# Performance work log

Measured on AMD Instinct MI355X. Metric: run time of the kernel, lower is better.

The kernel has to match this reference:

```python
import jax, jax.numpy as jnp
import numpy as np

N = 1024  # batch


def setup_inputs() -> dict:
    key = jax.random.key(0)
    ks = jax.random.split(key, 10)
    meta_feature = jax.random.uniform(ks[0], (N, 6), dtype=jnp.float32)
    tile_wall_feature = jax.random.uniform(ks[1], (N, 34, 5), dtype=jnp.float32)
    tile_prep = jax.random.uniform(ks[2], (N, 320, 34, 7), dtype=jnp.float32)
    # keep tile_hidden_ct (channel 4) away from 0 so the division stays well-conditioned
    tile_prep = tile_prep.at[..., 4].add(0.5)
    fan_prep = jax.random.uniform(ks[3], (N, 320, 80), dtype=jnp.float32)
    redundant_tile_prep = jax.random.uniform(ks[4], (N, 320, 34), dtype=jnp.float32)
    count_prep = jax.random.uniform(ks[5], (N, 320), dtype=jnp.float32)
    chi_peng_count_remain = jax.random.uniform(ks[6], (N, 320), dtype=jnp.float32)
    # learned params: Linear(11,1) of TileProbModuleNew, fan_coeff, tile_coeff
    W_throw = jax.random.normal(ks[7], (11,), dtype=jnp.float32) * 0.05
    b_throw = jnp.array(0.5, dtype=jnp.float32)  # keeps prob_throw > 0 (faithful math; avoids NaN from neg**frac)
    fan_coeff = 0.1 + 0.015 * jax.random.normal(ks[8], (80,), dtype=jnp.float32)
    tile_coeff = 1.0 + 0.015 * jax.random.normal(ks[9], (34,), dtype=jnp.float32)
    fan_coeff_multiplier = jnp.ones((80,), dtype=jnp.float32).at[33].set(21.0)
    return {
        'meta_feature': meta_feature,
        'tile_wall_feature': tile_wall_feature,
        'tile_prep': tile_prep,
        'fan_prep': fan_prep,
        'redundant_tile_prep': redundant_tile_prep,
        'count_prep': count_prep,
        'chi_peng_count_remain': chi_peng_count_remain,
        'W_throw': W_throw,
        'b_throw': b_throw,
        'fan_coeff': fan_coeff,
        'fan_coeff_multiplier': fan_coeff_multiplier,
        'tile_coeff': tile_coeff,
    }


def reference(meta_feature, tile_wall_feature, tile_prep, fan_prep,
              redundant_tile_prep, count_prep, chi_peng_count_remain,
              W_throw, b_throw, fan_coeff, fan_coeff_multiplier, tile_coeff):
    n = meta_feature.shape[0]
    # TileProbModuleNew: per-tile Linear(11,1)
    meta_exp = jnp.broadcast_to(meta_feature[:, None, :], (n, 34, 6))
    feat = jnp.concatenate([meta_exp, tile_wall_feature], axis=-1)        # (n,34,11)
    prob_throw = feat @ W_throw + b_throw                                  # (n,34)

    tile_self_draw_baseline = tile_prep[..., 0]
    tile_need_count = tile_prep[..., 1]
    tile_cp_coeff = tile_prep[..., 2]
    tile_cp_base = tile_prep[..., 3]
    tile_hidden_ct = tile_prep[..., 4]
    tile_cp_switch = tile_prep[..., 5]
    tile_null_filler = tile_prep[..., 6]

    fan_pref = fan_prep * fan_coeff * fan_coeff_multiplier                 # (n,320,80)
    multiplied_fan_pref = jnp.sum(fan_pref, axis=-1)                       # (n,320)

    term1 = tile_self_draw_baseline * prob_throw[:, None, :] ** tile_need_count
    term2 = jnp.nan_to_num(tile_cp_base * tile_cp_coeff / tile_hidden_ct)
    terms_summed = term1 + tile_null_filler + term2 * tile_cp_switch      # (n,320,34)

    final_prob_throw = jnp.prod(terms_summed, axis=-1) * 100.0 * multiplied_fan_pref  # (n,320)

    redundant_prob = redundant_tile_prep * final_prob_throw[..., None]    # (n,320,34)
    redundant_prob = redundant_prob.reshape(n, 5, 64, 34)
    tile_bound_winrate = redundant_prob.sum(axis=2)                        # (n,5,34)

    weighted_tile_prob = (tile_bound_winrate * tile_coeff)[:, 0]           # (n,34)

    final_prob_ops = final_prob_throw.reshape(n, 5, 64).sum(axis=-1)       # (n,5)
    max_tile_prob_for_action = jnp.max(tile_bound_winrate, axis=2)         # (n,5)
    max_tile_prob_for_action = max_tile_prob_for_action.at[:, 0].set(final_prob_ops[:, 0])
    return (max_tile_prob_for_action, weighted_tile_prob)
```

## Files before the change

### kernel.cpp

```cpp
#include <hip/hip_runtime.h>
#include <math.h>

#define N_OPS 320

__global__ __launch_bounds__(256) void mahjong_kernel(
    const float* __restrict__ meta,
    const float* __restrict__ wall,
    const float* __restrict__ tile_prep,
    const float* __restrict__ fan_prep,
    const float* __restrict__ redundant,
    const float* __restrict__ W_throw,
    const float* __restrict__ b_throw,
    const float* __restrict__ fan_coeff,
    const float* __restrict__ fan_mult,
    const float* __restrict__ tile_coeff,
    float* __restrict__ out_max,
    float* __restrict__ out_weighted,
    int n)
{
    const int blk  = blockIdx.x;
    const int b    = blk / 5;
    const int g    = blk % 5;
    const int tid  = threadIdx.x;
    const int wave = tid >> 6;
    const int lane = tid & 63;

    __shared__ float terms_sm[32 * 34];
    __shared__ float qp_sm[32 * 21];
    __shared__ float prob_sm[34];
    __shared__ float fc_sm[80];
    __shared__ float final_sm[32];
    __shared__ float acc_sm[4][34];

    if (tid < 34) {
        float acc = b_throw[0];
        #pragma unroll
        for (int j = 0; j < 6; ++j) acc += meta[(size_t)b * 6 + j] * W_throw[j];
        const float* w = wall + ((size_t)b * 34 + tid) * 5;
        #pragma unroll
        for (int j = 0; j < 5; ++j) acc += w[j] * W_throw[6 + j];
        prob_sm[tid] = acc;
    }
    if (tid >= 64 && tid < 144) {
        int f = tid - 64;
        fc_sm[f] = fan_coeff[f] * fan_mult[f];
    }
    __syncthreads();

    float acc3 = 0.0f;
    float fsum_part = 0.0f;

    const int t_init = tid % 34;

    for (int c = 0; c < 2; ++c) {
        const size_t row0 = (size_t)b * N_OPS + g * 64 + c * 32;

        if (c) __syncthreads();

        {
            const float* tp0 = tile_prep + row0 * 238;
            int t = t_init;
            #pragma unroll
            for (int k = 0; k < 4; ++k) {
                const int tau = tid + 256 * k;
                const float* e = tp0 + 7 * tau;
                float c0 = e[0], c1 = e[1], c2 = e[2], c3 = e[3];
                float c4 = e[4], c5 = e[5], c6 = e[6];
                float term = c0 * exp2f(c1 * log2f(prob_sm[t])) + c6 + (c3 * c2 / c4) * c5;
                terms_sm[tau] = term;
                t += 18; if (t >= 34) t -= 34;
            }
            if (tid < 64) {
                const int tau = 1024 + tid;
                int t2 = tid + 4;
                if (t2 >= 34) t2 -= 34;
                if (t2 >= 34) t2 -= 34;
                const float* e = tp0 + 7 * tau;
                float c0 = e[0], c1 = e[1], c2 = e[2], c3 = e[3];
                float c4 = e[4], c5 = e[5], c6 = e[6];
                float term = c0 * exp2f(c1 * log2f(prob_sm[t2])) + c6 + (c3 * c2 / c4) * c5;
                terms_sm[tau] = term;
            }
        }

        {
            const float4* fsrc = (const float4*)(fan_prep + row0 * 80);
            #pragma unroll
            for (int k = 0; k < 3; ++k) {
                const int i = tid + 256 * k;
                if (i < 640) {
                    float4 v = fsrc[i];
                    const int r = i / 20;
                    const int q = i - r * 20;
                    const int f = 4 * q;
                    qp_sm[r * 21 + q] = v.x * fc_sm[f]     + v.y * fc_sm[f + 1]
                                      + v.z * fc_sm[f + 2] + v.w * fc_sm[f + 3];
                }
            }
        }
        __syncthreads();

        if (tid < 32) {
            const float* tr = terms_sm + tid * 34;
            float p = 1.0f;
            #pragma unroll
            for (int t = 0; t < 34; ++t) p *= tr[t];
            const float* qr = qp_sm + tid * 21;
            float q = 0.0f;
            #pragma unroll
            for (int j = 0; j < 20; ++j) q += qr[j];
            float fin = p * 100.0f * q;
            final_sm[tid] = fin;
            fsum_part += fin;
        }
        __syncthreads();

        if (lane < 34) {
            const float* rr0 = redundant + (row0 + wave * 8) * 34;
            #pragma unroll
            for (int i = 0; i < 8; ++i)
                acc3 += rr0[i * 34 + lane] * final_sm[wave * 8 + i];
        }
    }

    if (lane < 34) acc_sm[wave][lane] = acc3;
    __syncthreads();

    if (wave == 0) {
        float tbw = 0.0f;
        if (lane < 34)
            tbw = acc_sm[0][lane] + acc_sm[1][lane] + acc_sm[2][lane] + acc_sm[3][lane];
        if (g == 0) {
            if (lane < 34)
                out_weighted[(size_t)b * 34 + lane] = tbw * tile_coeff[lane];
            float fs = fsum_part;
            #pragma unroll
            for (int sh = 1; sh < 64; sh <<= 1) fs += __shfl_xor(fs, sh);
            if (lane == 0) out_max[(size_t)b * 5] = fs;
        } else {
            float m = (lane < 34) ? tbw : -INFINITY;
            #pragma unroll
            for (int sh = 1; sh < 64; sh <<= 1) m = fmaxf(m, __shfl_xor(m, sh));
            if (lane == 0) out_max[(size_t)b * 5 + g] = m;
        }
    }
}

extern "C" void kernel_launch(void* const* d_in, const int* in_sizes, int n_in,
                              void* d_out, int out_size, void* d_ws, size_t ws_size,
                              hipStream_t stream) {
    const float* meta       = (const float*)d_in[0];
    const float* wall       = (const float*)d_in[1];
    const float* tile_prep  = (const float*)d_in[2];
    const float* fan_prep   = (const float*)d_in[3];
    const float* redundant  = (const float*)d_in[4];
    const float* W_throw    = (const float*)d_in[7];
    const float* b_throw    = (const float*)d_in[8];
    const float* fan_coeff  = (const float*)d_in[9];
    const float* fan_mult   = (const float*)d_in[10];
    const float* tile_coeff = (const float*)d_in[11];

    int n = in_sizes[0] / 6;
    float* out_max      = (float*)d_out;
    float* out_weighted = out_max + (size_t)n * 5;

    dim3 grid(n * 5), block(256);
    hipLaunchKernelGGL(mahjong_kernel, grid, block, 0, stream,
                       meta, wall, tile_prep, fan_prep, redundant,
                       W_throw, b_throw, fan_coeff, fan_mult, tile_coeff,
                       out_max, out_weighted, n);
}
```

Baseline: 510.9 us.

## Stage tile_prep through shared memory with float4 loads and per-row shuffle products

Each 16-row chunk of tile_prep is now copied into shared memory with coalesced float4 loads, replacing per-thread strided scalar loads of 7 channels. The term computation is then split so 16 threads share one row, each covering 2-3 tiles. The 34-way product and the fan sum are reduced with warp shuffles instead of a single-thread serial loop. The redundant-weighted accumulation is deferred until all chunks finish, which removes one barrier per chunk but adds more chunks (4 instead of 2) and therefore more barriers.

New measurement: 517.6 us. About the same (+1.3%).

```diff
diff --git a/kernel.cpp b/kernel.cpp
--- a/kernel.cpp
+++ b/kernel.cpp
@@ -2,6 +2,9 @@
 #include <math.h>
 
 #define N_OPS 320
+#define RPC 16
+#define NCHUNK 4
+#define F4_PER_CHUNK 952
 
 __global__ __launch_bounds__(256) void mahjong_kernel(
     const float* __restrict__ meta,
@@ -25,12 +28,12 @@
     const int wave = tid >> 6;
     const int lane = tid & 63;
 
-    __shared__ float terms_sm[32 * 34];
-    __shared__ float qp_sm[32 * 21];
-    __shared__ float prob_sm[34];
-    __shared__ float fc_sm[80];
-    __shared__ float final_sm[32];
-    __shared__ float acc_sm[4][34];
+    __shared__ float4 stage4[F4_PER_CHUNK];
+    __shared__ float  qp_sm[RPC * 20];
+    __shared__ float  prob_sm[34];
+    __shared__ float  fc_sm[80];
+    __shared__ float  final_sm[64];
+    __shared__ float  acc_sm[4][34];
 
     if (tid < 34) {
         float acc = b_throw[0];
@@ -47,83 +50,65 @@
     }
     __syncthreads();
 
-    float acc3 = 0.0f;
-    float fsum_part = 0.0f;
+    const int r = tid >> 4;
+    const int p = tid & 15;
+    const int tcount = (p < 2) ? 3 : 2;
+    const int t0     = (p < 2) ? 3 * p : 2 * p + 2;
 
-    const int t_init = tid % 34;
+    const size_t rowB = (size_t)b * N_OPS + g * 64;
 
-    for (int c = 0; c < 2; ++c) {
-        const size_t row0 = (size_t)b * N_OPS + g * 64 + c * 32;
+    for (int c = 0; c < NCHUNK; ++c) {
+        const size_t row0 = rowB + c * RPC;
 
-        if (c) __syncthreads();
-
-        {
-            const float* tp0 = tile_prep + row0 * 238;
-            int t = t_init;
-            #pragma unroll
-            for (int k = 0; k < 4; ++k) {
-                const int tau = tid + 256 * k;
-                const float* e = tp0 + 7 * tau;
-                float c0 = e[0], c1 = e[1], c2 = e[2], c3 = e[3];
-                float c4 = e[4], c5 = e[5], c6 = e[6];
-                float term = c0 * exp2f(c1 * log2f(prob_sm[t])) + c6 + (c3 * c2 / c4) * c5;
-                terms_sm[tau] = term;
-                t += 18; if (t >= 34) t -= 34;
-            }
-            if (tid < 64) {
-                const int tau = 1024 + tid;
-                int t2 = tid + 4;
-                if (t2 >= 34) t2 -= 34;
-                if (t2 >= 34) t2 -= 34;
-                const float* e = tp0 + 7 * tau;
-                float c0 = e[0], c1 = e[1], c2 = e[2], c3 = e[3];
-                float c4 = e[4], c5 = e[5], c6 = e[6];
-                float term = c0 * exp2f(c1 * log2f(prob_sm[t2])) + c6 + (c3 * c2 / c4) * c5;
-                terms_sm[tau] = term;
-            }
-        }
+        const float4* src4 = (const float4*)(tile_prep + row0 * 238);
+        #pragma unroll
+        for (int k = 0; k < 3; ++k) stage4[tid + 256 * k] = src4[tid + 256 * k];
+        if (tid < F4_PER_CHUNK - 768) stage4[tid + 768] = src4[tid + 768];
 
         {
             const float4* fsrc = (const float4*)(fan_prep + row0 * 80);
-            #pragma unroll
-            for (int k = 0; k < 3; ++k) {
-                const int i = tid + 256 * k;
-                if (i < 640) {
-                    float4 v = fsrc[i];
-                    const int r = i / 20;
-                    const int q = i - r * 20;
-                    const int f = 4 * q;
-                    qp_sm[r * 21 + q] = v.x * fc_sm[f]     + v.y * fc_sm[f + 1]
-                                      + v.z * fc_sm[f + 2] + v.w * fc_sm[f + 3];
-                }
+            float4 v = fsrc[tid];
+            int f = 4 * (tid % 20);
+            qp_sm[tid] = v.x * fc_sm[f]     + v.y * fc_sm[f + 1]
+                       + v.z * fc_sm[f + 2] + v.w * fc_sm[f + 3];
+            if (tid < RPC * 20 - 256) {
+                int i = 256 + tid;
+                float4 u = fsrc[i];
+                int f2 = 4 * (i % 20);
+                qp_sm[i] = u.x * fc_sm[f2]     + u.y * fc_sm[f2 + 1]
+                         + u.z * fc_sm[f2 + 2] + u.w * fc_sm[f2 + 3];
             }
         }
         __syncthreads();
 
-        if (tid < 32) {
-            const float* tr = terms_sm + tid * 34;
-            float p = 1.0f;
-            #pragma unroll
-            for (int t = 0; t < 34; ++t) p *= tr[t];
-            const float* qr = qp_sm + tid * 21;
-            float q = 0.0f;
-            #pragma unroll
-            for (int j = 0; j < 20; ++j) q += qr[j];
-            float fin = p * 100.0f * q;
-            final_sm[tid] = fin;
-            fsum_part += fin;
+        const float* srow = (const float*)stage4 + r * 238;
+        float prod = 1.0f;
+        for (int ti = 0; ti < tcount; ++ti) {
+            const int t = t0 + ti;
+            const float* e = srow + 7 * t;
+            float c0 = e[0], c1 = e[1], c2 = e[2], c3 = e[3];
+            float c4 = e[4], c5 = e[5], c6 = e[6];
+            prod *= c0 * exp2f(c1 * log2f(prob_sm[t])) + c6 + (c3 * c2 / c4) * c5;
         }
+        const float* qr = qp_sm + r * 20;
+        float qs = (p < 4) ? (qr[2 * p] + qr[2 * p + 1]) : qr[4 + p];
+        #pragma unroll
+        for (int sh = 1; sh < 16; sh <<= 1) {
+            prod *= __shfl_xor(prod, sh);
+            qs   += __shfl_xor(qs, sh);
+        }
+        if (p == 0) final_sm[c * RPC + r] = prod * 100.0f * qs;
         __syncthreads();
-
-        if (lane < 34) {
-            const float* rr0 = redundant + (row0 + wave * 8) * 34;
-            #pragma unroll
-            for (int i = 0; i < 8; ++i)
-                acc3 += rr0[i * 34 + lane] * final_sm[wave * 8 + i];
-        }
     }
 
-    if (lane < 34) acc_sm[wave][lane] = acc3;
+    if (lane < 34) {
+        const float* rr = redundant + (rowB + wave * 16) * 34;
+        float acc3 = 0.0f;
+        #pragma unroll
+        for (int i = 0; i < 16; ++i)
+            acc3 += rr[i * 34 + lane] * final_sm[wave * 16 + i];
+        acc_sm[wave][lane] = acc3;
+    }
     __syncthreads();
 
     if (wave == 0) {
@@ -133,7 +118,7 @@
         if (g == 0) {
             if (lane < 34)
                 out_weighted[(size_t)b * 34 + lane] = tbw * tile_coeff[lane];
-            float fs = fsum_part;
+            float fs = final_sm[lane];
             #pragma unroll
             for (int sh = 1; sh < 64; sh <<= 1) fs += __shfl_xor(fs, sh);
             if (lane == 0) out_max[(size_t)b * 5] = fs;
```
